# Performance work log

Hardware: AMD Instinct MI355X
Metric: run time of the kernel (lower is better)

Reference implementation:

```python
import jax, jax.numpy as jnp
import numpy as np

N = 50000      # nodes
E = 800000     # edges (avg degree 16)
SIZES = [128, 128, 128, 128, 64]
NUM_LAYERS = 4


def setup_inputs() -> dict:
    key = jax.random.key(0)
    ks = jax.random.split(key, 3 + 2 * NUM_LAYERS)
    inp = {
        "x": jax.random.normal(ks[0], (N, SIZES[0]), dtype=jnp.float32),
        "edge_index": jax.random.randint(ks[1], (2, E), 0, N, dtype=jnp.int64),
        "edge_weight": jax.random.uniform(ks[2], (E,), dtype=jnp.float32),
    }
    for i in range(NUM_LAYERS):
        fan_in = SIZES[i]
        inp[f"W{i}"] = (jax.random.normal(ks[3 + 2 * i], (SIZES[i], SIZES[i + 1]), dtype=jnp.float32)
                        / np.float32(np.sqrt(fan_in)))
        inp[f"b{i}"] = jnp.zeros((SIZES[i + 1],), dtype=jnp.float32)
    return inp


def gcn_conv(x, src, dst, ew, W, b, n):
    """PyG GCNConv with add_self_loops=True, normalize=True (eval mode).
    deg[i] = sum of incoming edge weights at i + 1 (self loop weight 1).
    norm(j->i) = deg[j]^-1/2 * w_ji * deg[i]^-1/2.
    Self loop contributes deg[i]^-1 * (xW)[i].
    """
    xw = x @ W                                                    # [n, out]
    deg = jax.ops.segment_sum(ew, dst, num_segments=n) + 1.0      # [n]
    dinv = jnp.where(deg > 0, jax.lax.rsqrt(deg), 0.0)            # deg^-1/2
    norm = dinv[src] * ew * dinv[dst]                             # [E]
    agg = jax.ops.segment_sum(xw[src] * norm[:, None], dst, num_segments=n)
    return agg + xw * (dinv * dinv)[:, None] + b


def reference(x, edge_index, edge_weight, W0, b0, W1, b1, W2, b2, W3, b3):
    # Dropout p=0.5 is identity in eval mode (training=False).
    src, dst = edge_index[0], edge_index[1]
    Ws = [W0, W1, W2, W3]
    bs = [b0, b1, b2, b3]
    for i in range(NUM_LAYERS):
        x = gcn_conv(x, src, dst, edge_weight, Ws[i], bs[i], N)
        if i < NUM_LAYERS - 1:
            x = jax.nn.relu(x)
    return x
```

## Files before the change

kernel.cpp:

```cpp
#include <hip/hip_runtime.h>
#include <hip/hip_fp16.h>


#define DEG_SCALE 4194304.0f
#define BCAP 5120
#define K1_EDGES 4096
#define ACT_LD 136

using f16x8 = __attribute__((ext_vector_type(8))) _Float16;
using f32x4 = __attribute__((ext_vector_type(4))) float;

__global__ void prep_kernel(const float* __restrict__ W0, const float* __restrict__ W1,
                            const float* __restrict__ W2, const float* __restrict__ W3,
                            __half* P0, __half* P1, __half* P2, __half* P3,
                            int* gCursor, int nBuckets) {
    int blk = blockIdx.x;
    if (blk == 28) {
        int t = threadIdx.x;
        if (t < nBuckets) gCursor[t] = t * BCAP;
        return;
    }
    int t = blk * 256 + threadIdx.x;
    const float* W;
    __half* P;
    int OUT;
    if (t < 2048)      { W = W0; P = P0; OUT = 128; }
    else if (t < 4096) { W = W1; P = P1; OUT = 128; t -= 2048; }
    else if (t < 6144) { W = W2; P = P2; OUT = 128; t -= 4096; }
    else               { W = W3; P = P3; OUT = 64;  t -= 6144; }
    int lane = t & 63, fi = t >> 6;
    int nt = fi >> 2, kc = fi & 3;
    int col = 16 * nt + (lane & 15);
    int k0  = 32 * kc + 8 * (lane >> 4);
    union { __half h[8]; uint4 u; } v;
#pragma unroll
    for (int j = 0; j < 8; j++) v.h[j] = __float2half_rn(W[(size_t)(k0 + j) * OUT + col]);
    *(uint4*)&P[((size_t)fi * 64 + lane) * 8] = v.u;
}

__global__ __launch_bounds__(256) void bucket_scatter_kernel(
        const int* __restrict__ src, const int* __restrict__ dst,
        const float* __restrict__ ew, int* gCursor,
        int2* __restrict__ bucketArr, int E, int nBuckets) {
    __shared__ int cnt[256];
    __shared__ int runBase[256];
    int tid = threadIdx.x;
    int e0 = blockIdx.x * K1_EDGES;
    int e1 = min(e0 + K1_EDGES, E);
    cnt[tid] = 0;
    __syncthreads();
    for (int e = e0 + tid; e < e1; e += 256)
        atomicAdd(&cnt[dst[e] >> 8], 1);
    __syncthreads();
    if (tid < nBuckets && cnt[tid] > 0)
        runBase[tid] = atomicAdd(&gCursor[tid], cnt[tid]);
    __syncthreads();
    cnt[tid] = 0;
    __syncthreads();
    for (int e = e0 + tid; e < e1; e += 256) {
        int d = dst[e];
        int b = d >> 8;
        int slot = runBase[b] + atomicAdd(&cnt[b], 1);
        if (slot < (b + 1) * BCAP)
            bucketArr[slot] = make_int2((src[e] & 0xFFFF) | (d << 16),
                                        __float_as_int(ew[e]));
    }
}

__global__ __launch_bounds__(256) void bucket_csr_kernel(
        const int2* __restrict__ bucketArr, const int* __restrict__ gCursor,
        int2* __restrict__ epack, int* __restrict__ row_ptr,
        float* __restrict__ dinv, int N, int E, int nBuckets) {
    __shared__ int2 st[BCAP];
    __shared__ int cnt[256];
    __shared__ int scn[256];
    __shared__ int cur[256];
    __shared__ unsigned int dfix[256];
    __shared__ int cbase_sh;
    int b   = blockIdx.x;
    int tid = threadIdx.x;
    int node0 = b << 8;
    int nloc  = min(256, N - node0);
    int base  = b * BCAP;

    int sz = (tid < nBuckets) ? (gCursor[tid] - tid * BCAP) : 0;
    scn[tid] = sz;
    __syncthreads();
    for (int off = 1; off < 256; off <<= 1) {
        int u = (tid >= off) ? scn[tid - off] : 0;
        __syncthreads();
        scn[tid] += u;
        __syncthreads();
    }
    if (tid == b) cbase_sh = scn[tid] - sz;
    cnt[tid]  = 0;
    dfix[tid] = 0u;
    __syncthreads();
    int cbase = cbase_sh;
    int size  = gCursor[b] - base;

    for (int i = tid; i < size; i += 256) {
        int2 v = bucketArr[base + i];
        st[i] = v;
        int dl = (v.x >> 16) & 255;
        atomicAdd(&cnt[dl], 1);
        atomicAdd(&dfix[dl], (unsigned int)rintf(__int_as_float(v.y) * DEG_SCALE));
    }
    __syncthreads();

    if (tid < nloc) {
        float d = (float)dfix[tid] * (1.0f / DEG_SCALE) + 1.0f;
        dinv[node0 + tid] = rsqrtf(d);
    }

    int val = cnt[tid];
    scn[tid] = val;
    __syncthreads();
    for (int off = 1; off < 256; off <<= 1) {
        int u = (tid >= off) ? scn[tid - off] : 0;
        __syncthreads();
        scn[tid] += u;
        __syncthreads();
    }
    int excl = scn[tid] - val;
    scn[tid] = excl;
    if (tid < nloc) row_ptr[node0 + tid] = cbase + excl;
    if (b == nBuckets - 1 && tid == 0) row_ptr[N] = E;
    cur[tid] = 0;
    __syncthreads();

    for (int i = tid; i < size; i += 256) {
        int2 v = st[i];
        int dl = (v.x >> 16) & 255;
        int p  = cbase + scn[dl] + atomicAdd(&cur[dl], 1);
        epack[p] = make_int2(v.x & 0xFFFF, v.y);
    }
}

__global__ __launch_bounds__(256) void gemm0_kernel(const float* __restrict__ x,
                                                    const __half* __restrict__ Wpack,
                                                    const float* __restrict__ dinv,
                                                    __half* __restrict__ xw, int nrows) {
    constexpr int OUT = 128, NT = 8, CPR = 16;
    __shared__ __half D[64 * OUT];
    int tid  = threadIdx.x;
    int wave = tid >> 6, lane = tid & 63;
    int r = lane & 15, g = lane >> 4;
    int row0 = blockIdx.x * 64 + wave * 16;

    int arow = row0 + r;
    if (arow >= nrows) arow = nrows - 1;

    f16x8 a[4];
#pragma unroll
    for (int kc = 0; kc < 4; kc++) {
        const float* p = x + (size_t)arow * 128 + kc * 32 + g * 8;
        float4 u = *(const float4*)p;
        float4 v = *(const float4*)(p + 4);
        a[kc][0] = (_Float16)u.x; a[kc][1] = (_Float16)u.y;
        a[kc][2] = (_Float16)u.z; a[kc][3] = (_Float16)u.w;
        a[kc][4] = (_Float16)v.x; a[kc][5] = (_Float16)v.y;
        a[kc][6] = (_Float16)v.z; a[kc][7] = (_Float16)v.w;
    }

    float4 dv = *(const float4*)&dinv[row0 + 4 * g];

#pragma unroll
    for (int nt = 0; nt < NT; nt++) {
        const f16x8* Bp = (const f16x8*)(Wpack) + (size_t)nt * 4 * 64 + lane;
        f32x4 c = {0.f, 0.f, 0.f, 0.f};
        c = __builtin_amdgcn_mfma_f32_16x16x32_f16(a[0], Bp[0],   c, 0, 0, 0);
        c = __builtin_amdgcn_mfma_f32_16x16x32_f16(a[1], Bp[64],  c, 0, 0, 0);
        c = __builtin_amdgcn_mfma_f32_16x16x32_f16(a[2], Bp[128], c, 0, 0, 0);
        c = __builtin_amdgcn_mfma_f32_16x16x32_f16(a[3], Bp[192], c, 0, 0, 0);
        c[0] *= dv.x; c[1] *= dv.y; c[2] *= dv.z; c[3] *= dv.w;
        int col = 16 * nt + r;
#pragma unroll
        for (int j = 0; j < 4; j++) {
            int drow = wave * 16 + 4 * g + j;
            int ch   = (col >> 3) ^ (drow & (CPR - 1));
            D[drow * OUT + ch * 8 + (col & 7)] = __float2half_rn(c[j]);
        }
    }
    __syncthreads();
#pragma unroll
    for (int i = 0; i < 4; i++) {
        int idx  = tid + i * 256;
        int drow = idx / CPR;
        int ch   = idx % CPR;
        int gr   = blockIdx.x * 64 + drow;
        if (gr < nrows) {
            f16x8 v = *(f16x8*)&D[drow * OUT + ((ch ^ (drow & (CPR - 1))) << 3)];
            *(f16x8*)&xw[(size_t)gr * OUT + ch * 8] = v;
        }
    }
}

template <int OUT_NEXT>
__global__ __launch_bounds__(256) void gather_gemm_kernel(
        const __half* __restrict__ xwh,
        const int* __restrict__ rp,
        const int2* __restrict__ epack,
        const float* __restrict__ dinv,
        const float* __restrict__ bias,
        const __half* __restrict__ Wpack,
        __half* __restrict__ xw_out,
        int n) {
    constexpr int NT  = OUT_NEXT / 16;
    constexpr int NTW = NT / 4;
    constexpr int CPR = OUT_NEXT / 8;
    __shared__ __half act[16 * ACT_LD];
    __shared__ __half D[16 * OUT_NEXT];
    int tid  = threadIdx.x;
    int wv   = tid >> 6, lane = tid & 63;
    int node0 = blockIdx.x * 16;

#pragma unroll
    for (int k = 0; k < 4; k++) {
        int lrow = wv * 4 + k;
        int node = node0 + lrow;
        if (node < n) {
            node = __builtin_amdgcn_readfirstlane(node);
            int e0 = rp[node], e1 = rp[node + 1];
            float ax = 0.f, ay = 0.f;
            int e = e0;
            for (; e + 16 <= e1; e += 16) {
                int2 v[16];
#pragma unroll
                for (int j = 0; j < 16; j++) v[j] = epack[e + j];
                __half2 h[16];
#pragma unroll
                for (int j = 0; j < 16; j++)
                    h[j] = ((const __half2*)(xwh + (size_t)v[j].x * 128))[lane];
#pragma unroll
                for (int j = 0; j < 16; j++) {
                    float w = __int_as_float(v[j].y);
                    ax += __half2float(h[j].x) * w;
                    ay += __half2float(h[j].y) * w;
                }
            }
            for (; e + 4 <= e1; e += 4) {
                int2 v[4];
#pragma unroll
                for (int j = 0; j < 4; j++) v[j] = epack[e + j];
                __half2 h[4];
#pragma unroll
                for (int j = 0; j < 4; j++)
                    h[j] = ((const __half2*)(xwh + (size_t)v[j].x * 128))[lane];
#pragma unroll
                for (int j = 0; j < 4; j++) {
                    float w = __int_as_float(v[j].y);
                    ax += __half2float(h[j].x) * w;
                    ay += __half2float(h[j].y) * w;
                }
            }
            for (; e < e1; e++) {
                int2 v = epack[e];
                __half2 h = ((const __half2*)(xwh + (size_t)v.x * 128))[lane];
                float w = __int_as_float(v.y);
                ax += __half2float(h.x) * w;
                ay += __half2float(h.y) * w;
            }
            float   dvn = dinv[node];
            __half2 hs  = ((const __half2*)(xwh + (size_t)node * 128))[lane];
            float2  bl  = *(const float2*)&bias[lane * 2];
            float ox = fmaxf(dvn * (ax + __half2float(hs.x)) + bl.x, 0.f);
            float oy = fmaxf(dvn * (ay + __half2float(hs.y)) + bl.y, 0.f);
            __half2 ho;
            ho.x = __float2half_rn(ox);
            ho.y = __float2half_rn(oy);
            *(__half2*)&act[lrow * ACT_LD + lane * 2] = ho;
        }
    }
    __syncthreads();

    int r = lane & 15, g = lane >> 4;
    f16x8 a[4];
#pragma unroll
    for (int kc = 0; kc < 4; kc++)
        a[kc] = *(const f16x8*)&act[r * ACT_LD + kc * 32 + g * 8];

    float4 dvw = *(const float4*)&dinv[node0 + 4 * g];

#pragma unroll
    for (int t = 0; t < NTW; t++) {
        int nt = wv * NTW + t;
        const f16x8* Bp = (const f16x8*)(Wpack) + (size_t)nt * 4 * 64 + lane;
        f32x4 c = {0.f, 0.f, 0.f, 0.f};
        c = __builtin_amdgcn_mfma_f32_16x16x32_f16(a[0], Bp[0],   c, 0, 0, 0);
        c = __builtin_amdgcn_mfma_f32_16x16x32_f16(a[1], Bp[64],  c, 0, 0, 0);
        c = __builtin_amdgcn_mfma_f32_16x16x32_f16(a[2], Bp[128], c, 0, 0, 0);
        c = __builtin_amdgcn_mfma_f32_16x16x32_f16(a[3], Bp[192], c, 0, 0, 0);
        c[0] *= dvw.x; c[1] *= dvw.y; c[2] *= dvw.z; c[3] *= dvw.w;
        int col = 16 * nt + r;
#pragma unroll
        for (int j = 0; j < 4; j++) {
            int drow = 4 * g + j;
            int ch   = (col >> 3) ^ (drow & (CPR - 1));
            D[drow * OUT_NEXT + ch * 8 + (col & 7)] = __float2half_rn(c[j]);
        }
    }
    __syncthreads();

    constexpr int CHUNKS = 16 * CPR;
    if (tid < CHUNKS) {
        int drow = tid / CPR;
        int ch   = tid % CPR;
        int gr   = node0 + drow;
        if (gr < n) {
            f16x8 v = *(f16x8*)&D[drow * OUT_NEXT + ((ch ^ (drow & (CPR - 1))) << 3)];
            *(f16x8*)&xw_out[(size_t)gr * OUT_NEXT + ch * 8] = v;
        }
    }
}

__global__ __launch_bounds__(256) void gather64h_kernel(const __half* __restrict__ xwh,
                                                        const int* __restrict__ rp,
                                                        const int2* __restrict__ epack,
                                                        const float* __restrict__ dinv,
                                                        const float* __restrict__ bias,
                                                        float* __restrict__ out, int n) {
    int lane = threadIdx.x & 63;
    int node = (blockIdx.x * blockDim.x + threadIdx.x) >> 6;
    if (node >= n) return;
    node = __builtin_amdgcn_readfirstlane(node);
    int e0 = rp[node], e1 = rp[node + 1];
    float acc = 0.f;

    int e = e0;
    for (; e + 16 <= e1; e += 16) {
        int2 v[16];
#pragma unroll
        for (int j = 0; j < 16; j++) v[j] = epack[e + j];
        __half h[16];
#pragma unroll
        for (int j = 0; j < 16; j++) h[j] = xwh[(size_t)v[j].x * 64 + lane];
#pragma unroll
        for (int j = 0; j < 16; j++)
            acc += __half2float(h[j]) * __int_as_float(v[j].y);
    }
    for (; e + 4 <= e1; e += 4) {
        int2 v[4];
#pragma unroll
        for (int j = 0; j < 4; j++) v[j] = epack[e + j];
        __half h[4];
#pragma unroll
        for (int j = 0; j < 4; j++) h[j] = xwh[(size_t)v[j].x * 64 + lane];
#pragma unroll
        for (int j = 0; j < 4; j++)
            acc += __half2float(h[j]) * __int_as_float(v[j].y);
    }
    for (; e < e1; e++) {
        int2 v = epack[e];
        acc += __half2float(xwh[(size_t)v.x * 64 + lane]) * __int_as_float(v.y);
    }

    float self = __half2float(xwh[(size_t)node * 64 + lane]);
    out[(size_t)node * 64 + lane] = dinv[node] * (acc + self) + bias[lane];
}

extern "C" void kernel_launch(void* const* d_in, const int* in_sizes, int n_in,
                              void* d_out, int out_size, void* d_ws, size_t ws_size,
                              hipStream_t stream) {
    const float* x  = (const float*)d_in[0];
    const int*   ei = (const int*)d_in[1];
    const float* ew = (const float*)d_in[2];
    const float* W[4] = {(const float*)d_in[3], (const float*)d_in[5],
                         (const float*)d_in[7], (const float*)d_in[9]};
    const float* b[4] = {(const float*)d_in[4], (const float*)d_in[6],
                         (const float*)d_in[8], (const float*)d_in[10]};
    const int N = in_sizes[0] / 128;
    const int E = in_sizes[2];
    const int* srcIdx = ei;
    const int* dstIdx = ei + E;
    float* out = (float*)d_out;

    const int nBuckets = (N + 255) / 256;

    char* p = (char*)d_ws;
    auto alloc = [&](size_t bytes) -> char* {
        char* q = p;
        p += (bytes + 255) / 256 * 256;
        return q;
    };
    float*  dinv      = (float*)alloc((size_t)(N + 64) * 4);
    int*    row_ptr   = (int*)alloc((size_t)(N + 1) * 4);
    int*    gCursor   = (int*)alloc(256 * 4);
    int2*   bucketArr = (int2*)alloc((size_t)nBuckets * BCAP * 8);
    int2*   epack     = (int2*)alloc((size_t)E * 8);
    __half* xwA       = (__half*)alloc((size_t)N * 128 * 2);
    __half* xwB       = (__half*)alloc((size_t)N * 128 * 2);
    __half* Wp[4];
    Wp[0] = (__half*)alloc(128 * 128 * 2);
    Wp[1] = (__half*)alloc(128 * 128 * 2);
    Wp[2] = (__half*)alloc(128 * 128 * 2);
    Wp[3] = (__half*)alloc(128 * 64 * 2);

    const int k1_grid    = (E + K1_EDGES - 1) / K1_EDGES;
    const int gemm_grid  = (N + 63) / 64;
    const int fused_grid = (N + 15) / 16;
    const int g64_grid   = (N + 3) / 4;

    prep_kernel<<<29, 256, 0, stream>>>(W[0], W[1], W[2], W[3],
                                        Wp[0], Wp[1], Wp[2], Wp[3],
                                        gCursor, nBuckets);
    bucket_scatter_kernel<<<k1_grid, 256, 0, stream>>>(srcIdx, dstIdx, ew, gCursor,
                                                       bucketArr, E, nBuckets);
    bucket_csr_kernel<<<nBuckets, 256, 0, stream>>>(bucketArr, gCursor, epack,
                                                    row_ptr, dinv, N, E, nBuckets);
    gemm0_kernel<<<gemm_grid, 256, 0, stream>>>(x, Wp[0], dinv, xwA, N);
    gather_gemm_kernel<128><<<fused_grid, 256, 0, stream>>>(
        xwA, row_ptr, epack, dinv, b[0], Wp[1], xwB, N);
    gather_gemm_kernel<128><<<fused_grid, 256, 0, stream>>>(
        xwB, row_ptr, epack, dinv, b[1], Wp[2], xwA, N);
    gather_gemm_kernel<64><<<fused_grid, 256, 0, stream>>>(
        xwA, row_ptr, epack, dinv, b[2], Wp[3], xwB, N);
    gather64h_kernel<<<g64_grid, 256, 0, stream>>>(
        xwB, row_ptr, epack, dinv, b[3], out, N);
}
```

Baseline: 185.8 us.

## Slice CSR rows by source-index range for gather cache locality

Each node's edges are sub-sorted into 8 slices by source index, giving a per-slice row pointer array. The fused gather kernels walk all four of a wave's nodes slice by slice, so nodes processed at the same time read source rows from the same 8K-node window, aiming to improve L2 hit rate on xw gathers. In exchange, the row pointer array grows eightfold, each node needs more loop overhead and pointer loads, and the 16-wide unrolled gather loop is removed.

```diff
diff --git a/kernel.cpp b/kernel.cpp
--- a/kernel.cpp
+++ b/kernel.cpp
@@ -6,6 +6,8 @@
 #define BCAP 5120
 #define K1_EDGES 4096
 #define ACT_LD 136
+#define NSLICE 8
+#define SLICE_SHIFT 13
 
 using f16x8 = __attribute__((ext_vector_type(8))) _Float16;
 using f32x4 = __attribute__((ext_vector_type(4))) float;
@@ -69,12 +71,12 @@
 
 __global__ __launch_bounds__(256) void bucket_csr_kernel(
         const int2* __restrict__ bucketArr, const int* __restrict__ gCursor,
-        int2* __restrict__ epack, int* __restrict__ row_ptr,
+        int2* __restrict__ epack, int* __restrict__ rp2,
         float* __restrict__ dinv, int N, int E, int nBuckets) {
     __shared__ int2 st[BCAP];
-    __shared__ int cnt[256];
+    __shared__ int cnt2[256 * NSLICE];
+    __shared__ int offs[256 * NSLICE];
     __shared__ int scn[256];
-    __shared__ int cur[256];
     __shared__ unsigned int dfix[256];
     __shared__ int cbase_sh;
     int b   = blockIdx.x;
@@ -93,7 +95,8 @@
         __syncthreads();
     }
     if (tid == b) cbase_sh = scn[tid] - sz;
-    cnt[tid]  = 0;
+#pragma unroll
+    for (int s = 0; s < NSLICE; s++) cnt2[tid * NSLICE + s] = 0;
     dfix[tid] = 0u;
     __syncthreads();
     int cbase = cbase_sh;
@@ -103,7 +106,8 @@
         int2 v = bucketArr[base + i];
         st[i] = v;
         int dl = (v.x >> 16) & 255;
-        atomicAdd(&cnt[dl], 1);
+        int sl = (v.x & 0xFFFF) >> SLICE_SHIFT;
+        atomicAdd(&cnt2[dl * NSLICE + sl], 1);
         atomicAdd(&dfix[dl], (unsigned int)rintf(__int_as_float(v.y) * DEG_SCALE));
     }
     __syncthreads();
@@ -113,8 +117,10 @@
         dinv[node0 + tid] = rsqrtf(d);
     }
 
-    int val = cnt[tid];
-    scn[tid] = val;
+    int tot = 0;
+#pragma unroll
+    for (int s = 0; s < NSLICE; s++) tot += cnt2[tid * NSLICE + s];
+    scn[tid] = tot;
     __syncthreads();
     for (int off = 1; off < 256; off <<= 1) {
         int u = (tid >= off) ? scn[tid - off] : 0;
@@ -122,17 +128,26 @@
         scn[tid] += u;
         __syncthreads();
     }
-    int excl = scn[tid] - val;
-    scn[tid] = excl;
-    if (tid < nloc) row_ptr[node0 + tid] = cbase + excl;
-    if (b == nBuckets - 1 && tid == 0) row_ptr[N] = E;
-    cur[tid] = 0;
+    int run = cbase + scn[tid] - tot;
+    if (tid < nloc) {
+#pragma unroll
+        for (int s = 0; s < NSLICE; s++) {
+            offs[tid * NSLICE + s] = run;
+            rp2[(size_t)(node0 + tid) * NSLICE + s] = run;
+            run += cnt2[tid * NSLICE + s];
+        }
+    }
+    if (b == nBuckets - 1 && tid == 0) rp2[(size_t)N * NSLICE] = E;
+    __syncthreads();
+#pragma unroll
+    for (int s = 0; s < NSLICE; s++) cnt2[tid * NSLICE + s] = 0;
     __syncthreads();
 
     for (int i = tid; i < size; i += 256) {
         int2 v = st[i];
         int dl = (v.x >> 16) & 255;
-        int p  = cbase + scn[dl] + atomicAdd(&cur[dl], 1);
+        int sl = (v.x & 0xFFFF) >> SLICE_SHIFT;
+        int p  = offs[dl * NSLICE + sl] + atomicAdd(&cnt2[dl * NSLICE + sl], 1);
         epack[p] = make_int2(v.x & 0xFFFF, v.y);
     }
 }
@@ -199,7 +214,7 @@
 template <int OUT_NEXT>
 __global__ __launch_bounds__(256) void gather_gemm_kernel(
         const __half* __restrict__ xwh,
-        const int* __restrict__ rp,
+        const int* __restrict__ rp2,
         const int2* __restrict__ epack,
         const float* __restrict__ dinv,
         const float* __restrict__ bias,
@@ -214,31 +229,19 @@
     int tid  = threadIdx.x;
     int wv   = tid >> 6, lane = tid & 63;
     int node0 = blockIdx.x * 16;
-
-#pragma unroll
-    for (int k = 0; k < 4; k++) {
-        int lrow = wv * 4 + k;
-        int node = node0 + lrow;
-        if (node < n) {
-            node = __builtin_amdgcn_readfirstlane(node);
-            int e0 = rp[node], e1 = rp[node + 1];
-            float ax = 0.f, ay = 0.f;
+    int nbase = node0 + wv * 4;
+
+    float ax[4] = {0.f, 0.f, 0.f, 0.f};
+    float ay[4] = {0.f, 0.f, 0.f, 0.f};
+
+    for (int s = 0; s < NSLICE; s++) {
+#pragma unroll
+        for (int k = 0; k < 4; k++) {
+            int node = nbase + k;
+            if (node >= n) continue;
+            int e0 = rp2[(size_t)node * NSLICE + s];
+            int e1 = rp2[(size_t)node * NSLICE + s + 1];
             int e = e0;
-            for (; e + 16 <= e1; e += 16) {
-                int2 v[16];
-#pragma unroll
-                for (int j = 0; j < 16; j++) v[j] = epack[e + j];
-                __half2 h[16];
-#pragma unroll
-                for (int j = 0; j < 16; j++)
-                    h[j] = ((const __half2*)(xwh + (size_t)v[j].x * 128))[lane];
-#pragma unroll
-                for (int j = 0; j < 16; j++) {
-                    float w = __int_as_float(v[j].y);
-                    ax += __half2float(h[j].x) * w;
-                    ay += __half2float(h[j].y) * w;
-                }
-            }
             for (; e + 4 <= e1; e += 4) {
                 int2 v[4];
 #pragma unroll
@@ -250,22 +253,29 @@
 #pragma unroll
                 for (int j = 0; j < 4; j++) {
                     float w = __int_as_float(v[j].y);
-                    ax += __half2float(h[j].x) * w;
-                    ay += __half2float(h[j].y) * w;
+                    ax[k] += __half2float(h[j].x) * w;
+                    ay[k] += __half2float(h[j].y) * w;
                 }
             }
             for (; e < e1; e++) {
                 int2 v = epack[e];
                 __half2 h = ((const __half2*)(xwh + (size_t)v.x * 128))[lane];
                 float w = __int_as_float(v.y);
-                ax += __half2float(h.x) * w;
-                ay += __half2float(h.y) * w;
+                ax[k] += __half2float(h.x) * w;
+                ay[k] += __half2float(h.y) * w;
             }
+        }
+    }
+#pragma unroll
+    for (int k = 0; k < 4; k++) {
+        int node = nbase + k;
+        if (node < n) {
+            int lrow = wv * 4 + k;
             float   dvn = dinv[node];
             __half2 hs  = ((const __half2*)(xwh + (size_t)node * 128))[lane];
             float2  bl  = *(const float2*)&bias[lane * 2];
-            float ox = fmaxf(dvn * (ax + __half2float(hs.x)) + bl.x, 0.f);
-            float oy = fmaxf(dvn * (ay + __half2float(hs.y)) + bl.y, 0.f);
+            float ox = fmaxf(dvn * (ax[k] + __half2float(hs.x)) + bl.x, 0.f);
+            float oy = fmaxf(dvn * (ay[k] + __half2float(hs.y)) + bl.y, 0.f);
             __half2 ho;
             ho.x = __float2half_rn(ox);
             ho.y = __float2half_rn(oy);
@@ -315,7 +325,7 @@
 }
 
 __global__ __launch_bounds__(256) void gather64h_kernel(const __half* __restrict__ xwh,
-                                                        const int* __restrict__ rp,
+                                                        const int* __restrict__ rp2,
                                                         const int2* __restrict__ epack,
                                                         const float* __restrict__ dinv,
                                                         const float* __restrict__ bias,
@@ -324,7 +334,8 @@
     int node = (blockIdx.x * blockDim.x + threadIdx.x) >> 6;
     if (node >= n) return;
     node = __builtin_amdgcn_readfirstlane(node);
-    int e0 = rp[node], e1 = rp[node + 1];
+    int e0 = rp2[(size_t)node * NSLICE];
+    int e1 = rp2[(size_t)(node + 1) * NSLICE];
     float acc = 0.f;
 
     int e = e0;
@@ -384,7 +395,7 @@
         return q;
     };
     float*  dinv      = (float*)alloc((size_t)(N + 64) * 4);
-    int*    row_ptr   = (int*)alloc((size_t)(N + 1) * 4);
+    int*    rp2       = (int*)alloc(((size_t)N * NSLICE + 1) * 4);
     int*    gCursor   = (int*)alloc(256 * 4);
     int2*   bucketArr = (int2*)alloc((size_t)nBuckets * BCAP * 8);
     int2*   epack     = (int2*)alloc((size_t)E * 8);
@@ -407,14 +418,14 @@
     bucket_scatter_kernel<<<k1_grid, 256, 0, stream>>>(srcIdx, dstIdx, ew, gCursor,
                                                        bucketArr, E, nBuckets);
     bucket_csr_kernel<<<nBuckets, 256, 0, stream>>>(bucketArr, gCursor, epack,
-                                                    row_ptr, dinv, N, E, nBuckets);
+                                                    rp2, dinv, N, E, nBuckets);
     gemm0_kernel<<<gemm_grid, 256, 0, stream>>>(x, Wp[0], dinv, xwA, N);
     gather_gemm_kernel<128><<<fused_grid, 256, 0, stream>>>(
-        xwA, row_ptr, epack, dinv, b[0], Wp[1], xwB, N);
+        xwA, rp2, epack, dinv, b[0], Wp[1], xwB, N);
     gather_gemm_kernel<128><<<fused_grid, 256, 0, stream>>>(
-        xwB, row_ptr, epack, dinv, b[1], Wp[2], xwA, N);
+        xwB, rp2, epack, dinv, b[1], Wp[2], xwA, N);
     gather_gemm_kernel<64><<<fused_grid, 256, 0, stream>>>(
-        xwA, row_ptr, epack, dinv, b[2], Wp[3], xwB, N);
+        xwA, rp2, epack, dinv, b[2], Wp[3], xwB, N);
     gather64h_kernel<<<g64_grid, 256, 0, stream>>>(
-        xwB, row_ptr, epack, dinv, b[3], out, N);
-}
+        xwB, rp2, epack, dinv, b[3], out, N);
+}
```

Result: slower. 379.1 us (+104.0%).

## Split fused gather+GEMM kernels into separate gather and GEMM launches

Applied to the files above, without the earlier changes.

Replaces the fused per-layer gather-then-MFMA kernel (16 nodes per block, 4 nodes per wave) with a standalone gather kernel that writes activations to a global fp16 buffer, followed by a generic templated MFMA GEMM kernel. The gather kernel now uses one wave per node with full occupancy and no shared-memory staging. The intent is to decouple the latency-bound irregular gather from the compute phase so each can use its best launch shape. In exchange it adds an extra global round trip of an N x 128 fp16 activation tensor per layer and three more kernel launches.

```diff
diff --git a/kernel.cpp b/kernel.cpp
--- a/kernel.cpp
+++ b/kernel.cpp
@@ -5,7 +5,6 @@
 #define DEG_SCALE 4194304.0f
 #define BCAP 5120
 #define K1_EDGES 4096
-#define ACT_LD 136
 
 using f16x8 = __attribute__((ext_vector_type(8))) _Float16;
 using f32x4 = __attribute__((ext_vector_type(4))) float;
@@ -137,11 +136,13 @@
     }
 }
 
-__global__ __launch_bounds__(256) void gemm0_kernel(const float* __restrict__ x,
-                                                    const __half* __restrict__ Wpack,
-                                                    const float* __restrict__ dinv,
-                                                    __half* __restrict__ xw, int nrows) {
-    constexpr int OUT = 128, NT = 8, CPR = 16;
+template <int OUT, bool AFP32>
+__global__ __launch_bounds__(256) void gemm_kernel(const void* __restrict__ A,
+                                                   const __half* __restrict__ Wpack,
+                                                   const float* __restrict__ dinv,
+                                                   __half* __restrict__ xw, int nrows) {
+    constexpr int NT  = OUT / 16;
+    constexpr int CPR = OUT / 8;
     __shared__ __half D[64 * OUT];
     int tid  = threadIdx.x;
     int wave = tid >> 6, lane = tid & 63;
@@ -154,13 +155,17 @@
     f16x8 a[4];
 #pragma unroll
     for (int kc = 0; kc < 4; kc++) {
-        const float* p = x + (size_t)arow * 128 + kc * 32 + g * 8;
-        float4 u = *(const float4*)p;
-        float4 v = *(const float4*)(p + 4);
-        a[kc][0] = (_Float16)u.x; a[kc][1] = (_Float16)u.y;
-        a[kc][2] = (_Float16)u.z; a[kc][3] = (_Float16)u.w;
-        a[kc][4] = (_Float16)v.x; a[kc][5] = (_Float16)v.y;
-        a[kc][6] = (_Float16)v.z; a[kc][7] = (_Float16)v.w;
+        if (AFP32) {
+            const float* p = (const float*)A + (size_t)arow * 128 + kc * 32 + g * 8;
+            float4 u = *(const float4*)p;
+            float4 v = *(const float4*)(p + 4);
+            a[kc][0] = (_Float16)u.x; a[kc][1] = (_Float16)u.y;
+            a[kc][2] = (_Float16)u.z; a[kc][3] = (_Float16)u.w;
+            a[kc][4] = (_Float16)v.x; a[kc][5] = (_Float16)v.y;
+            a[kc][6] = (_Float16)v.z; a[kc][7] = (_Float16)v.w;
+        } else {
+            a[kc] = *(const f16x8*)((const __half*)A + (size_t)arow * 128 + kc * 32 + g * 8);
+        }
     }
 
     float4 dv = *(const float4*)&dinv[row0 + 4 * g];
@@ -184,7 +189,7 @@
     }
     __syncthreads();
 #pragma unroll
-    for (int i = 0; i < 4; i++) {
+    for (int i = 0; i < 64 * CPR / 256; i++) {
         int idx  = tid + i * 256;
         int drow = idx / CPR;
         int ch   = idx % CPR;
@@ -196,122 +201,67 @@
     }
 }
 
-template <int OUT_NEXT>
-__global__ __launch_bounds__(256) void gather_gemm_kernel(
-        const __half* __restrict__ xwh,
-        const int* __restrict__ rp,
-        const int2* __restrict__ epack,
-        const float* __restrict__ dinv,
-        const float* __restrict__ bias,
-        const __half* __restrict__ Wpack,
-        __half* __restrict__ xw_out,
-        int n) {
-    constexpr int NT  = OUT_NEXT / 16;
-    constexpr int NTW = NT / 4;
-    constexpr int CPR = OUT_NEXT / 8;
-    __shared__ __half act[16 * ACT_LD];
-    __shared__ __half D[16 * OUT_NEXT];
-    int tid  = threadIdx.x;
-    int wv   = tid >> 6, lane = tid & 63;
-    int node0 = blockIdx.x * 16;
-
-#pragma unroll
-    for (int k = 0; k < 4; k++) {
-        int lrow = wv * 4 + k;
-        int node = node0 + lrow;
-        if (node < n) {
-            node = __builtin_amdgcn_readfirstlane(node);
-            int e0 = rp[node], e1 = rp[node + 1];
-            float ax = 0.f, ay = 0.f;
-            int e = e0;
-            for (; e + 16 <= e1; e += 16) {
-                int2 v[16];
-#pragma unroll
-                for (int j = 0; j < 16; j++) v[j] = epack[e + j];
-                __half2 h[16];
-#pragma unroll
-                for (int j = 0; j < 16; j++)
-                    h[j] = ((const __half2*)(xwh + (size_t)v[j].x * 128))[lane];
-#pragma unroll
-                for (int j = 0; j < 16; j++) {
-                    float w = __int_as_float(v[j].y);
-                    ax += __half2float(h[j].x) * w;
-                    ay += __half2float(h[j].y) * w;
-                }
-            }
-            for (; e + 4 <= e1; e += 4) {
-                int2 v[4];
-#pragma unroll
-                for (int j = 0; j < 4; j++) v[j] = epack[e + j];
-                __half2 h[4];
-#pragma unroll
-                for (int j = 0; j < 4; j++)
-                    h[j] = ((const __half2*)(xwh + (size_t)v[j].x * 128))[lane];
-#pragma unroll
-                for (int j = 0; j < 4; j++) {
-                    float w = __int_as_float(v[j].y);
-                    ax += __half2float(h[j].x) * w;
-                    ay += __half2float(h[j].y) * w;
-                }
-            }
-            for (; e < e1; e++) {
-                int2 v = epack[e];
-                __half2 h = ((const __half2*)(xwh + (size_t)v.x * 128))[lane];
-                float w = __int_as_float(v.y);
-                ax += __half2float(h.x) * w;
-                ay += __half2float(h.y) * w;
-            }
-            float   dvn = dinv[node];
-            __half2 hs  = ((const __half2*)(xwh + (size_t)node * 128))[lane];
-            float2  bl  = *(const float2*)&bias[lane * 2];
-            float ox = fmaxf(dvn * (ax + __half2float(hs.x)) + bl.x, 0.f);
-            float oy = fmaxf(dvn * (ay + __half2float(hs.y)) + bl.y, 0.f);
-            __half2 ho;
-            ho.x = __float2half_rn(ox);
-            ho.y = __float2half_rn(oy);
-            *(__half2*)&act[lrow * ACT_LD + lane * 2] = ho;
-        }
-    }
-    __syncthreads();
-
-    int r = lane & 15, g = lane >> 4;
-    f16x8 a[4];
-#pragma unroll
-    for (int kc = 0; kc < 4; kc++)
-        a[kc] = *(const f16x8*)&act[r * ACT_LD + kc * 32 + g * 8];
-
-    float4 dvw = *(const float4*)&dinv[node0 + 4 * g];
-
-#pragma unroll
-    for (int t = 0; t < NTW; t++) {
-        int nt = wv * NTW + t;
-        const f16x8* Bp = (const f16x8*)(Wpack) + (size_t)nt * 4 * 64 + lane;
-        f32x4 c = {0.f, 0.f, 0.f, 0.f};
-        c = __builtin_amdgcn_mfma_f32_16x16x32_f16(a[0], Bp[0],   c, 0, 0, 0);
-        c = __builtin_amdgcn_mfma_f32_16x16x32_f16(a[1], Bp[64],  c, 0, 0, 0);
-        c = __builtin_amdgcn_mfma_f32_16x16x32_f16(a[2], Bp[128], c, 0, 0, 0);
-        c = __builtin_amdgcn_mfma_f32_16x16x32_f16(a[3], Bp[192], c, 0, 0, 0);
-        c[0] *= dvw.x; c[1] *= dvw.y; c[2] *= dvw.z; c[3] *= dvw.w;
-        int col = 16 * nt + r;
+__global__ __launch_bounds__(256) void gather128_kernel(const __half* __restrict__ xwh,
+                                                        const int* __restrict__ rp,
+                                                        const int2* __restrict__ epack,
+                                                        const float* __restrict__ dinv,
+                                                        const float* __restrict__ bias,
+                                                        __half* __restrict__ act, int n) {
+    int lane = threadIdx.x & 63;
+    int node = (blockIdx.x * blockDim.x + threadIdx.x) >> 6;
+    if (node >= n) return;
+    node = __builtin_amdgcn_readfirstlane(node);
+    int e0 = rp[node], e1 = rp[node + 1];
+    float ax = 0.f, ay = 0.f;
+
+    int e = e0;
+    for (; e + 16 <= e1; e += 16) {
+        int2 v[16];
+#pragma unroll
+        for (int j = 0; j < 16; j++) v[j] = epack[e + j];
+        __half2 h[16];
+#pragma unroll
+        for (int j = 0; j < 16; j++)
+            h[j] = ((const __half2*)(xwh + (size_t)v[j].x * 128))[lane];
+#pragma unroll
+        for (int j = 0; j < 16; j++) {
+            float w = __int_as_float(v[j].y);
+            ax += __half2float(h[j].x) * w;
+            ay += __half2float(h[j].y) * w;
+        }
+    }
+    for (; e + 4 <= e1; e += 4) {
+        int2 v[4];
+#pragma unroll
+        for (int j = 0; j < 4; j++) v[j] = epack[e + j];
+        __half2 h[4];
+#pragma unroll
+        for (int j = 0; j < 4; j++)
+            h[j] = ((const __half2*)(xwh + (size_t)v[j].x * 128))[lane];
 #pragma unroll
         for (int j = 0; j < 4; j++) {
-            int drow = 4 * g + j;
-            int ch   = (col >> 3) ^ (drow & (CPR - 1));
-            D[drow * OUT_NEXT + ch * 8 + (col & 7)] = __float2half_rn(c[j]);
-        }
-    }
-    __syncthreads();
-
-    constexpr int CHUNKS = 16 * CPR;
-    if (tid < CHUNKS) {
-        int drow = tid / CPR;
-        int ch   = tid % CPR;
-        int gr   = node0 + drow;
-        if (gr < n) {
-            f16x8 v = *(f16x8*)&D[drow * OUT_NEXT + ((ch ^ (drow & (CPR - 1))) << 3)];
-            *(f16x8*)&xw_out[(size_t)gr * OUT_NEXT + ch * 8] = v;
-        }
-    }
+            float w = __int_as_float(v[j].y);
+            ax += __half2float(h[j].x) * w;
+            ay += __half2float(h[j].y) * w;
+        }
+    }
+    for (; e < e1; e++) {
+        int2 v = epack[e];
+        __half2 h = ((const __half2*)(xwh + (size_t)v.x * 128))[lane];
+        float w = __int_as_float(v.y);
+        ax += __half2float(h.x) * w;
+        ay += __half2float(h.y) * w;
+    }
+
+    float   dvn = dinv[node];
+    __half2 hs  = ((const __half2*)(xwh + (size_t)node * 128))[lane];
+    float2  bl  = *(const float2*)&bias[lane * 2];
+    float ox = fmaxf(dvn * (ax + __half2float(hs.x)) + bl.x, 0.f);
+    float oy = fmaxf(dvn * (ay + __half2float(hs.y)) + bl.y, 0.f);
+    __half2 ho;
+    ho.x = __float2half_rn(ox);
+    ho.y = __float2half_rn(oy);
+    *(__half2*)&act[(size_t)node * 128 + lane * 2] = ho;
 }
 
 __global__ __launch_bounds__(256) void gather64h_kernel(const __half* __restrict__ xwh,
@@ -390,16 +340,16 @@
     int2*   epack     = (int2*)alloc((size_t)E * 8);
     __half* xwA       = (__half*)alloc((size_t)N * 128 * 2);
     __half* xwB       = (__half*)alloc((size_t)N * 128 * 2);
+    __half* act       = (__half*)alloc((size_t)N * 128 * 2);
     __half* Wp[4];
     Wp[0] = (__half*)alloc(128 * 128 * 2);
     Wp[1] = (__half*)alloc(128 * 128 * 2);
     Wp[2] = (__half*)alloc(128 * 128 * 2);
     Wp[3] = (__half*)alloc(128 * 64 * 2);
 
-    const int k1_grid    = (E + K1_EDGES - 1) / K1_EDGES;
-    const int gemm_grid  = (N + 63) / 64;
-    const int fused_grid = (N + 15) / 16;
-    const int g64_grid   = (N + 3) / 4;
+    const int k1_grid     = (E + K1_EDGES - 1) / K1_EDGES;
+    const int gemm_grid   = (N + 63) / 64;
+    const int gather_grid = (N + 3) / 4;
 
     prep_kernel<<<29, 256, 0, stream>>>(W[0], W[1], W[2], W[3],
                                         Wp[0], Wp[1], Wp[2], Wp[3],
@@ -408,13 +358,17 @@
                                                        bucketArr, E, nBuckets);
     bucket_csr_kernel<<<nBuckets, 256, 0, stream>>>(bucketArr, gCursor, epack,
                                                     row_ptr, dinv, N, E, nBuckets);
-    gemm0_kernel<<<gemm_grid, 256, 0, stream>>>(x, Wp[0], dinv, xwA, N);
-    gather_gemm_kernel<128><<<fused_grid, 256, 0, stream>>>(
-        xwA, row_ptr, epack, dinv, b[0], Wp[1], xwB, N);
-    gather_gemm_kernel<128><<<fused_grid, 256, 0, stream>>>(
-        xwB, row_ptr, epack, dinv, b[1], Wp[2], xwA, N);
-    gather_gemm_kernel<64><<<fused_grid, 256, 0, stream>>>(
-        xwA, row_ptr, epack, dinv, b[2], Wp[3], xwB, N);
-    gather64h_kernel<<<g64_grid, 256, 0, stream>>>(
-        xwB, row_ptr, epack, dinv, b[3], out, N);
-}
+
+    gemm_kernel<128, true><<<gemm_grid, 256, 0, stream>>>(x, Wp[0], dinv, xwA, N);
+    gather128_kernel<<<gather_grid, 256, 0, stream>>>(xwA, row_ptr, epack, dinv,
+                                                      b[0], act, N);
+    gemm_kernel<128, false><<<gemm_grid, 256, 0, stream>>>(act, Wp[1], dinv, xwB, N);
+    gather128_kernel<<<gather_grid, 256, 0, stream>>>(xwB, row_ptr, epack, dinv,
+                                                      b[1], act, N);
+    gemm_kernel<128, false><<<gemm_grid, 256, 0, stream>>>(act, Wp[2], dinv, xwA, N);
+    gather128_kernel<<<gather_grid, 256, 0, stream>>>(xwA, row_ptr, epack, dinv,
+                                                      b[2], act, N);
+    gemm_kernel<64, false><<<gemm_grid, 256, 0, stream>>>(act, Wp[3], dinv, xwB, N);
+    gather64h_kernel<<<gather_grid, 256, 0, stream>>>(xwB, row_ptr, epack, dinv,
+                                                      b[3], out, N);
+}
```

New measurement: 190.6 us. +2.6%, slower.
